# Kernel tuning notes

Measured on AMD Instinct MI355X. Metric: run time of the kernel, lower is better.

Reference implementation:

```python
import jax, jax.numpy as jnp
import numpy as np
from jax import lax

NEG = -9.0e15
ALPHA = 0.2  # LeakyReLU slope

def _cnn(x, conv1_w, conv1_b, conv2_w, conv2_b):
    # x: (BN,1,9,9)
    dn = ('NCHW', 'OIHW', 'NCHW')
    y = lax.conv_general_dilated(x, conv1_w, (1, 1), 'SAME', dimension_numbers=dn)
    y = jax.nn.relu(y + conv1_b[None, :, None, None])
    y = lax.conv_general_dilated(y, conv2_w, (1, 1), 'VALID', dimension_numbers=dn)
    y = jax.nn.relu(y + conv2_b[None, :, None, None])
    return y.reshape(y.shape[0], -1)  # (BN, 32*7*7=1568)

def _gat(h, adj, W, a1, a2):
    # h: (B,N,F) ; adj: (B,N,N) int
    Wh = h @ W                                  # (B,N,D)
    # a([Wh_i ; Wh_j]) == Wh_i@a1 + Wh_j@a2  (exact split of the concat linear)
    s1 = Wh @ a1                                # (B,N) query-node term
    s2 = Wh @ a2                                # (B,N) key-node term
    e = jax.nn.leaky_relu(s1[:, :, None] + s2[:, None, :], ALPHA)  # (B,N,N)
    e = jnp.where(adj > 0, e, NEG)
    attn = jax.nn.softmax(e, axis=-1)           # dropout off (eval mode)
    h_prime = jnp.einsum('bij,bjd->bid', attn, Wh)
    return jax.nn.elu(h_prime)

def reference(obs_grids, adj_matrix, conv1_w, conv1_b, conv2_w, conv2_b,
              W, a1, a2, actor_w, actor_b, critic_w, critic_b):
    B, N, C, H, Wd = obs_grids.shape
    feats = _cnn(obs_grids.reshape(B * N, C, H, Wd), conv1_w, conv1_b, conv2_w, conv2_b)
    feats = feats.reshape(B, N, -1)             # (B,N,1568)
    emb = _gat(feats, adj_matrix, W, a1, a2)    # (B,N,64)
    logits = emb @ actor_w + actor_b            # (B,N,n_actions)
    values = emb @ critic_w + critic_b          # (B,N,1)
    return (logits, values)

def setup_inputs() -> dict:
    key = jax.random.key(0)
    ks = jax.random.split(key, 12)
    B, N, H, Wd = 8, 1024, 9, 9
    FEAT, HID, NA = 1568, 64, 16
    f32 = jnp.float32
    inp = {}
    inp['obs_grids'] = jax.random.normal(ks[0], (B, N, 1, H, Wd), f32)
    inp['adj_matrix'] = jax.random.randint(ks[1], (B, N, N), 0, 2, jnp.int32)
    inp['conv1_w'] = jax.random.normal(ks[2], (16, 1, 3, 3), f32) * 0.1
    inp['conv1_b'] = jnp.zeros((16,), f32)
    inp['conv2_w'] = jax.random.normal(ks[3], (32, 16, 3, 3), f32) * 0.05
    inp['conv2_b'] = jnp.zeros((32,), f32)
    inp['W'] = jax.random.normal(ks[4], (FEAT, HID), f32) * (1.0 / np.sqrt(FEAT))
    inp['a1'] = jax.random.normal(ks[5], (HID,), f32) * 0.1
    inp['a2'] = jax.random.normal(ks[6], (HID,), f32) * 0.1
    inp['actor_w'] = jax.random.normal(ks[7], (HID, NA), f32) * (1.0 / np.sqrt(HID))
    inp['actor_b'] = jnp.zeros((NA,), f32)
    inp['critic_w'] = jax.random.normal(ks[8], (HID, 1), f32) * (1.0 / np.sqrt(HID))
    inp['critic_b'] = jnp.zeros((1,), f32)
    return inp
```

## Files before the change

kernel.cpp:

```cpp
#include <hip/hip_runtime.h>
#include <math.h>

#define NEG_BIG (-9.0e15f)

typedef __attribute__((ext_vector_type(8))) short short8;
typedef __attribute__((ext_vector_type(4))) float f32x4;

__device__ __forceinline__ short f32_to_bf16_bits(float f) {
  union { float f; unsigned u; } cv; cv.f = f;
  unsigned r = (cv.u + 0x7fffu + ((cv.u >> 16) & 1u)) >> 16;
  return (short)r;
}

__global__ __launch_bounds__(256) void wt_prep(const float* __restrict__ W,
                                               short* __restrict__ Wt) {
  int idx = blockIdx.x * 256 + threadIdx.x;
  if (idx < 1568 * 64) {
    int k = idx >> 6, n = idx & 63;
    Wt[n * 1568 + k] = f32_to_bf16_bits(W[idx]);
  }
}

#define IPB 8
#define FSTR 1608
__global__ __launch_bounds__(256) void cnn_gemm_kernel(
    const float* __restrict__ obs, const float* __restrict__ w1,
    const float* __restrict__ b1, const float* __restrict__ w2,
    const float* __restrict__ b2, const short* __restrict__ Wt,
    const float* __restrict__ a1, const float* __restrict__ a2,
    float* __restrict__ Wh, float* __restrict__ s1, float* __restrict__ s2)
{
  __shared__ float sw1[144];
  __shared__ float sb1[16];
  __shared__ float sb2[32];
  __shared__ __align__(16) short wt[32 * 160];
  __shared__ float sinp[IPB * 121];
  __shared__ __align__(16) short ubuf[IPB * FSTR];
  int tid = threadIdx.x;
  long inst0 = (long)blockIdx.x * IPB;

  for (int i = tid; i < 144; i += 256) sw1[i] = w1[i];
  if (tid < 16) sb1[tid] = b1[tid];
  if (tid < 32) sb2[tid] = b2[tid];
  for (int i = tid; i < 32 * 160; i += 256) {
    int o = i / 160, kp = i - o * 160;
    int kstep = kp >> 5, which = (kp >> 4) & 1, ci = kp & 15;
    int tap = kstep * 2 + which;
    float v = (tap < 9) ? w2[o * 144 + ci * 9 + tap] : 0.0f;
    wt[i] = f32_to_bf16_bits(v);
  }
  for (int i = tid; i < IPB * 121; i += 256) {
    int inst = i / 121, rem = i - inst * 121;
    int py = rem / 11, px = rem - py * 11;
    float v = 0.f;
    if (py >= 1 && py <= 9 && px >= 1 && px <= 9)
      v = obs[(inst0 + inst) * 81 + (py - 1) * 9 + (px - 1)];
    sinp[inst * 121 + rem] = v;
  }
  __syncthreads();

  {
    int inst = tid >> 5, s = tid & 31;
    const float* ib = &sinp[inst * 121];
    short* hw = &ubuf[inst * FSTR];
    for (int c = 0; c < 16; ++c) {
      float wk[9];
      #pragma unroll
      for (int k = 0; k < 9; ++k) wk[k] = sw1[c * 9 + k];
      float bias = sb1[c];
      #pragma unroll
      for (int t = 0; t < 3; ++t) {
        int px = s + t * 32;
        if (px < 81) {
          int y = (px * 456) >> 12;
          const float* ip = ib + px + 2 * y;
          float a = bias
            + ip[0]  * wk[0] + ip[1]  * wk[1] + ip[2]  * wk[2]
            + ip[11] * wk[3] + ip[12] * wk[4] + ip[13] * wk[5]
            + ip[22] * wk[6] + ip[23] * wk[7] + ip[24] * wk[8];
          a = fmaxf(a, 0.f);
          int idx = (px * 16 + c) ^ (((px >> 2) & 3) << 3);
          hw[idx] = f32_to_bf16_bits(a);
        }
      }
    }
  }

  int lane = tid & 63;
  int wv = tid >> 6;
  int g = lane >> 4;
  int which = g >> 1;
  int half = g & 1;
  int colr = lane & 15;

  const int offtab[9] = {0, 1, 2, 9, 10, 11, 18, 19, 20};
  int myoff[5];
  #pragma unroll
  for (int k = 0; k < 5; ++k) {
    int tap = k * 2 + which;
    myoff[k] = (tap < 9) ? offtab[tap] : 0;
  }
  int posm[4];
  #pragma unroll
  for (int mt = 0; mt < 4; ++mt) {
    int p = mt * 16 + colr;
    posm[mt] = (p < 49) ? (p / 7) * 9 + (p % 7) : 0;
  }
  short8 bfw[2][5];
  #pragma unroll
  for (int nt = 0; nt < 2; ++nt)
    #pragma unroll
    for (int k = 0; k < 5; ++k)
      bfw[nt][k] = *(const short8*)&wt[(nt * 16 + colr) * 160 + k * 32 + g * 8];

  #pragma unroll
  for (int ii = 0; ii < 2; ++ii) {
    int inst = wv * 2 + ii;
    const short* hb = &ubuf[inst * FSTR];
    short* fb = &ubuf[inst * FSTR];
    f32x4 acc[4][2];
    #pragma unroll
    for (int mt = 0; mt < 4; ++mt) {
      short8 af[5];
      #pragma unroll
      for (int k = 0; k < 5; ++k) {
        int row = posm[mt] + myoff[k];
        int idx = (row * 16 + half * 8) ^ (((row >> 2) & 3) << 3);
        af[k] = *(const short8*)&hb[idx];
      }
      #pragma unroll
      for (int nt = 0; nt < 2; ++nt) {
        f32x4 a0 = {0.f, 0.f, 0.f, 0.f};
        #pragma unroll
        for (int k = 0; k < 5; ++k)
          a0 = __builtin_amdgcn_mfma_f32_16x16x32_bf16(af[k], bfw[nt][k], a0, 0, 0, 0);
        acc[mt][nt] = a0;
      }
    }
    #pragma unroll
    for (int mt = 0; mt < 4; ++mt) {
      #pragma unroll
      for (int nt = 0; nt < 2; ++nt) {
        int o = nt * 16 + colr;
        float bias = sb2[o];
        #pragma unroll
        for (int r = 0; r < 4; ++r) {
          int p = mt * 16 + g * 4 + r;
          if (p < 49)
            fb[o * 49 + p] = f32_to_bf16_bits(fmaxf(acc[mt][nt][r] + bias, 0.f));
        }
      }
    }
  }
  __syncthreads();

  {
    int arow = colr & 7;
    const short* Wrow = Wt + (wv * 16 + colr) * 1568;
    f32x4 acc2 = {0.f, 0.f, 0.f, 0.f};
    for (int ks = 0; ks < 49; ++ks) {
      short8 af = *(const short8*)&ubuf[arow * FSTR + ks * 32 + g * 8];
      short8 bf = *(const short8*)&Wrow[ks * 32 + g * 8];
      acc2 = __builtin_amdgcn_mfma_f32_16x16x32_bf16(af, bf, acc2, 0, 0, 0);
    }
    float a1c = a1[wv * 16 + colr];
    float a2c = a2[wv * 16 + colr];
    float* sp1 = sinp;
    float* sp2 = sinp + 32;
    if (g < 2) {
      #pragma unroll
      for (int r = 0; r < 4; ++r) {
        int inst = g * 4 + r;
        float v = acc2[r];
        Wh[(inst0 + inst) * 64 + wv * 16 + colr] = v;
        float x1 = v * a1c, x2 = v * a2c;
        #pragma unroll
        for (int w = 1; w < 16; w <<= 1) { x1 += __shfl_xor(x1, w); x2 += __shfl_xor(x2, w); }
        if (colr == 0) { sp1[wv * 8 + inst] = x1; sp2[wv * 8 + inst] = x2; }
      }
    }
  }
  __syncthreads();
  if (tid < 8) {
    float* sp1 = sinp;
    float* sp2 = sinp + 32;
    s1[inst0 + tid] = sp1[tid] + sp1[8 + tid] + sp1[16 + tid] + sp1[24 + tid];
    s2[inst0 + tid] = sp2[tid] + sp2[8 + tid] + sp2[16 + tid] + sp2[24 + tid];
  }
}

#define PSTR 1028
__global__ __launch_bounds__(256) void gat_kernel(
    const int* __restrict__ adj, const float* __restrict__ Wh,
    const float* __restrict__ s1, const float* __restrict__ s2,
    const float* __restrict__ actor_w, const float* __restrict__ actor_b,
    const float* __restrict__ critic_w, const float* __restrict__ critic_b,
    float* __restrict__ out)
{
  __shared__ __align__(16) float p[16 * PSTR];
  __shared__ float s2s[1024];
  __shared__ float saw[64 * 16];
  __shared__ float scw[64];
  __shared__ float sab[16];
  __shared__ float denom[16];
  __shared__ float emb[16][65];
  int tid = threadIdx.x;
  int b = blockIdx.y;
  int i0 = blockIdx.x * 16;

  for (int j = tid; j < 1024; j += 256) s2s[j] = s2[b * 1024 + j];
  for (int idx2 = tid; idx2 < 64 * 16; idx2 += 256) saw[idx2] = actor_w[idx2];
  if (tid < 64) scw[tid] = critic_w[tid];
  if (tid < 16) sab[tid] = actor_b[tid];
  __syncthreads();

  {
    int il = tid >> 4, r = tid & 15;
    int i = i0 + il;
    float s1i = s1[b * 1024 + i];
    const int* arow = adj + ((long)(b * 1024 + i)) * 1024;
    float* prow = &p[il * PSTR];
    float m = -3.0e38f;
    for (int jj = 0; jj < 64; ++jj) {
      int j = r + jj * 16;
      int a = arow[j];
      float s = s1i + s2s[j];
      float e = (s > 0.f) ? s : 0.2f * s;
      e = (a > 0) ? e : NEG_BIG;
      prow[j] = e;
      m = fmaxf(m, e);
    }
    #pragma unroll
    for (int w = 1; w < 16; w <<= 1) m = fmaxf(m, __shfl_xor(m, w));
    float sum = 0.f;
    for (int jj = 0; jj < 64; ++jj) {
      int j = r + jj * 16;
      float pe = __expf(prow[j] - m);
      prow[j] = pe;
      sum += pe;
    }
    #pragma unroll
    for (int w = 1; w < 16; w <<= 1) sum += __shfl_xor(sum, w);
    if (r == 0) denom[il] = sum;
  }
  __syncthreads();

  int g = tid >> 6, sub = tid & 63, ti = sub >> 4, td = sub & 15;
  float acc[4][4] = {};
  const float* WhB = Wh + ((long)b * 1024) * 64;
  int k0 = g * 256;
  for (int k = k0; k < k0 + 256; k += 4) {
    float4 a4[4];
    #pragma unroll
    for (int ii = 0; ii < 4; ++ii) a4[ii] = *(const float4*)&p[(ti * 4 + ii) * PSTR + k];
    #pragma unroll
    for (int kk = 0; kk < 4; ++kk) {
      float4 wv2 = *(const float4*)&WhB[(k + kk) * 64 + td * 4];
      #pragma unroll
      for (int ii = 0; ii < 4; ++ii) {
        float av = (kk == 0) ? a4[ii].x : (kk == 1) ? a4[ii].y : (kk == 2) ? a4[ii].z : a4[ii].w;
        acc[ii][0] += av * wv2.x; acc[ii][1] += av * wv2.y;
        acc[ii][2] += av * wv2.z; acc[ii][3] += av * wv2.w;
      }
    }
  }
  __syncthreads();
  float* red = p;
  #pragma unroll
  for (int ii = 0; ii < 4; ++ii) {
    float4 v = {acc[ii][0], acc[ii][1], acc[ii][2], acc[ii][3]};
    *(float4*)&red[(g * 16 + ti * 4 + ii) * 64 + td * 4] = v;
  }
  __syncthreads();

  #pragma unroll
  for (int qq = 0; qq < 4; ++qq) {
    int q = tid + qq * 256;
    int il = q >> 6, d = q & 63;
    float v = red[il * 64 + d] + red[(16 + il) * 64 + d]
            + red[(32 + il) * 64 + d] + red[(48 + il) * 64 + d];
    v /= denom[il];
    v = (v > 0.f) ? v : expm1f(v);
    emb[il][d] = v;
  }
  __syncthreads();

  {
    int il = tid >> 4, na = tid & 15;
    float accl = sab[na];
    #pragma unroll
    for (int d = 0; d < 64; ++d) accl += emb[il][d] * saw[d * 16 + na];
    out[((long)(b * 1024 + i0 + il)) * 16 + na] = accl;
  }
  if (tid < 16) {
    float v = critic_b[0];
    #pragma unroll
    for (int d = 0; d < 64; ++d) v += emb[tid][d] * scw[d];
    out[131072 + b * 1024 + i0 + tid] = v;
  }
}

extern "C" void kernel_launch(void* const* d_in, const int* in_sizes, int n_in,
                              void* d_out, int out_size, void* d_ws, size_t ws_size,
                              hipStream_t stream)
{
  const float* obs = (const float*)d_in[0];
  const int*   adj = (const int*)d_in[1];
  const float* c1w = (const float*)d_in[2];
  const float* c1b = (const float*)d_in[3];
  const float* c2w = (const float*)d_in[4];
  const float* c2b = (const float*)d_in[5];
  const float* W   = (const float*)d_in[6];
  const float* a1  = (const float*)d_in[7];
  const float* a2  = (const float*)d_in[8];
  const float* aw  = (const float*)d_in[9];
  const float* ab  = (const float*)d_in[10];
  const float* cw  = (const float*)d_in[11];
  const float* cb  = (const float*)d_in[12];
  float* out = (float*)d_out;
  float* ws = (float*)d_ws;

  float* Wh  = ws;
  float* s1  = ws + 524288;
  float* s2  = s1 + 8192;
  short* Wt  = (short*)(s2 + 8192);

  hipLaunchKernelGGL(wt_prep, dim3((1568 * 64 + 255) / 256), dim3(256), 0, stream, W, Wt);
  hipLaunchKernelGGL(cnn_gemm_kernel, dim3(1024), dim3(256), 0, stream,
                     obs, c1w, c1b, c2w, c2b, Wt, a1, a2, Wh, s1, s2);
  hipLaunchKernelGGL(gat_kernel, dim3(64, 8), dim3(256), 0, stream,
                     adj, Wh, s1, s2, aw, ab, cw, cb, out);
}
```

Baseline: 80.19 us.

## Use bf16 MFMA for attention-weighted aggregation with transposed bf16 Wh

The CNN kernel now writes Wh as bf16 in a transposed (batch, feature, node) layout. The GAT kernel stores the softmax numerators as bf16 in shared memory and computes attn·Wh with 16x16x32 bf16 MFMA instead of the scalar FP32 outer-product loop and its cross-group reduction. The adjacency row is read with int4 loads into a per-thread bitmask and the logits are recomputed rather than staged in LDS. This halves Wh traffic and LDS use and removes a reduction pass, at the cost of bf16 rounding of the attention weights and Wh.

New measurement: 67.69 us. 1.18x faster.

```diff
diff --git a/kernel.cpp b/kernel.cpp
--- a/kernel.cpp
+++ b/kernel.cpp
@@ -4,6 +4,7 @@
 #define NEG_BIG (-9.0e15f)
 
 typedef __attribute__((ext_vector_type(8))) short short8;
+typedef __attribute__((ext_vector_type(4))) short short4v;
 typedef __attribute__((ext_vector_type(4))) float f32x4;
 
 __device__ __forceinline__ short f32_to_bf16_bits(float f) {
@@ -28,7 +29,7 @@
     const float* __restrict__ b1, const float* __restrict__ w2,
     const float* __restrict__ b2, const short* __restrict__ Wt,
     const float* __restrict__ a1, const float* __restrict__ a2,
-    float* __restrict__ Wh, float* __restrict__ s1, float* __restrict__ s2)
+    short* __restrict__ Whb, float* __restrict__ s1, float* __restrict__ s2)
 {
   __shared__ float sw1[144];
   __shared__ float sb1[16];
@@ -168,11 +169,16 @@
     float* sp1 = sinp;
     float* sp2 = sinp + 32;
     if (g < 2) {
+      long bidx = inst0 >> 10;
+      int node0 = (int)(inst0 & 1023) + g * 4;
+      short4v pk;
+      #pragma unroll
+      for (int r = 0; r < 4; ++r) pk[r] = f32_to_bf16_bits(acc2[r]);
+      *(short4v*)&Whb[(bidx * 64 + wv * 16 + colr) * 1024 + node0] = pk;
       #pragma unroll
       for (int r = 0; r < 4; ++r) {
         int inst = g * 4 + r;
         float v = acc2[r];
-        Wh[(inst0 + inst) * 64 + wv * 16 + colr] = v;
         float x1 = v * a1c, x2 = v * a2c;
         #pragma unroll
         for (int w = 1; w < 16; w <<= 1) { x1 += __shfl_xor(x1, w); x2 += __shfl_xor(x2, w); }
@@ -189,16 +195,16 @@
   }
 }
 
-#define PSTR 1028
+#define PSTR2 1096
 __global__ __launch_bounds__(256) void gat_kernel(
-    const int* __restrict__ adj, const float* __restrict__ Wh,
+    const int* __restrict__ adj, const short* __restrict__ Whb,
     const float* __restrict__ s1, const float* __restrict__ s2,
     const float* __restrict__ actor_w, const float* __restrict__ actor_b,
     const float* __restrict__ critic_w, const float* __restrict__ critic_b,
     float* __restrict__ out)
 {
-  __shared__ __align__(16) float p[16 * PSTR];
-  __shared__ float s2s[1024];
+  __shared__ __align__(16) short pb[16 * PSTR2];
+  __shared__ __align__(16) float s2s[1024];
   __shared__ float saw[64 * 16];
   __shared__ float scw[64];
   __shared__ float sab[16];
@@ -219,25 +225,43 @@
     int i = i0 + il;
     float s1i = s1[b * 1024 + i];
     const int* arow = adj + ((long)(b * 1024 + i)) * 1024;
-    float* prow = &p[il * PSTR];
+    unsigned long long amask = 0ull;
     float m = -3.0e38f;
-    for (int jj = 0; jj < 64; ++jj) {
-      int j = r + jj * 16;
-      int a = arow[j];
-      float s = s1i + s2s[j];
-      float e = (s > 0.f) ? s : 0.2f * s;
-      e = (a > 0) ? e : NEG_BIG;
-      prow[j] = e;
-      m = fmaxf(m, e);
+    #pragma unroll
+    for (int jj = 0; jj < 16; ++jj) {
+      int j0 = jj * 64 + r * 4;
+      int4 a4 = *(const int4*)&arow[j0];
+      float4 sv = *(const float4*)&s2s[j0];
+      float e0 = s1i + sv.x; e0 = (e0 > 0.f) ? e0 : 0.2f * e0;
+      float e1 = s1i + sv.y; e1 = (e1 > 0.f) ? e1 : 0.2f * e1;
+      float e2 = s1i + sv.z; e2 = (e2 > 0.f) ? e2 : 0.2f * e2;
+      float e3 = s1i + sv.w; e3 = (e3 > 0.f) ? e3 : 0.2f * e3;
+      if (a4.x > 0) { m = fmaxf(m, e0); amask |= 1ull << (jj * 4 + 0); }
+      if (a4.y > 0) { m = fmaxf(m, e1); amask |= 1ull << (jj * 4 + 1); }
+      if (a4.z > 0) { m = fmaxf(m, e2); amask |= 1ull << (jj * 4 + 2); }
+      if (a4.w > 0) { m = fmaxf(m, e3); amask |= 1ull << (jj * 4 + 3); }
     }
     #pragma unroll
     for (int w = 1; w < 16; w <<= 1) m = fmaxf(m, __shfl_xor(m, w));
     float sum = 0.f;
-    for (int jj = 0; jj < 64; ++jj) {
-      int j = r + jj * 16;
-      float pe = __expf(prow[j] - m);
-      prow[j] = pe;
-      sum += pe;
+    short* prow = &pb[il * PSTR2];
+    #pragma unroll
+    for (int jj = 0; jj < 16; ++jj) {
+      int j0 = jj * 64 + r * 4;
+      float4 sv = *(const float4*)&s2s[j0];
+      float e0 = s1i + sv.x; e0 = (e0 > 0.f) ? e0 : 0.2f * e0;
+      float e1 = s1i + sv.y; e1 = (e1 > 0.f) ? e1 : 0.2f * e1;
+      float e2 = s1i + sv.z; e2 = (e2 > 0.f) ? e2 : 0.2f * e2;
+      float e3 = s1i + sv.w; e3 = (e3 > 0.f) ? e3 : 0.2f * e3;
+      float p0 = ((amask >> (jj * 4 + 0)) & 1ull) ? __expf(e0 - m) : 0.f;
+      float p1 = ((amask >> (jj * 4 + 1)) & 1ull) ? __expf(e1 - m) : 0.f;
+      float p2 = ((amask >> (jj * 4 + 2)) & 1ull) ? __expf(e2 - m) : 0.f;
+      float p3 = ((amask >> (jj * 4 + 3)) & 1ull) ? __expf(e3 - m) : 0.f;
+      sum += (p0 + p1) + (p2 + p3);
+      short4v st;
+      st[0] = f32_to_bf16_bits(p0); st[1] = f32_to_bf16_bits(p1);
+      st[2] = f32_to_bf16_bits(p2); st[3] = f32_to_bf16_bits(p3);
+      *(short4v*)&prow[j0] = st;
     }
     #pragma unroll
     for (int w = 1; w < 16; w <<= 1) sum += __shfl_xor(sum, w);
@@ -245,43 +269,24 @@
   }
   __syncthreads();
 
-  int g = tid >> 6, sub = tid & 63, ti = sub >> 4, td = sub & 15;
-  float acc[4][4] = {};
-  const float* WhB = Wh + ((long)b * 1024) * 64;
-  int k0 = g * 256;
-  for (int k = k0; k < k0 + 256; k += 4) {
-    float4 a4[4];
-    #pragma unroll
-    for (int ii = 0; ii < 4; ++ii) a4[ii] = *(const float4*)&p[(ti * 4 + ii) * PSTR + k];
-    #pragma unroll
-    for (int kk = 0; kk < 4; ++kk) {
-      float4 wv2 = *(const float4*)&WhB[(k + kk) * 64 + td * 4];
-      #pragma unroll
-      for (int ii = 0; ii < 4; ++ii) {
-        float av = (kk == 0) ? a4[ii].x : (kk == 1) ? a4[ii].y : (kk == 2) ? a4[ii].z : a4[ii].w;
-        acc[ii][0] += av * wv2.x; acc[ii][1] += av * wv2.y;
-        acc[ii][2] += av * wv2.z; acc[ii][3] += av * wv2.w;
-      }
-    }
-  }
-  __syncthreads();
-  float* red = p;
-  #pragma unroll
-  for (int ii = 0; ii < 4; ++ii) {
-    float4 v = {acc[ii][0], acc[ii][1], acc[ii][2], acc[ii][3]};
-    *(float4*)&red[(g * 16 + ti * 4 + ii) * 64 + td * 4] = v;
-  }
-  __syncthreads();
-
-  #pragma unroll
-  for (int qq = 0; qq < 4; ++qq) {
-    int q = tid + qq * 256;
-    int il = q >> 6, d = q & 63;
-    float v = red[il * 64 + d] + red[(16 + il) * 64 + d]
-            + red[(32 + il) * 64 + d] + red[(48 + il) * 64 + d];
-    v /= denom[il];
-    v = (v > 0.f) ? v : expm1f(v);
-    emb[il][d] = v;
+  {
+    int lane = tid & 63, wv = tid >> 6, g = lane >> 4, colr = lane & 15;
+    const short* Wcol = Whb + ((long)b * 64 + wv * 16 + colr) * 1024;
+    const short* prow = &pb[colr * PSTR2];
+    f32x4 acc = {0.f, 0.f, 0.f, 0.f};
+    #pragma unroll
+    for (int ks = 0; ks < 32; ++ks) {
+      short8 af = *(const short8*)&prow[ks * 32 + g * 8];
+      short8 bf = *(const short8*)&Wcol[ks * 32 + g * 8];
+      acc = __builtin_amdgcn_mfma_f32_16x16x32_bf16(af, bf, acc, 0, 0, 0);
+    }
+    #pragma unroll
+    for (int rr = 0; rr < 4; ++rr) {
+      int row = g * 4 + rr;
+      float v = acc[rr] / denom[row];
+      v = (v > 0.f) ? v : expm1f(v);
+      emb[row][wv * 16 + colr] = v;
+    }
   }
   __syncthreads();
 
@@ -320,14 +325,14 @@
   float* out = (float*)d_out;
   float* ws = (float*)d_ws;
 
-  float* Wh  = ws;
-  float* s1  = ws + 524288;
+  short* Whb = (short*)ws;
+  float* s1  = ws + 262144;
   float* s2  = s1 + 8192;
   short* Wt  = (short*)(s2 + 8192);
 
   hipLaunchKernelGGL(wt_prep, dim3((1568 * 64 + 255) / 256), dim3(256), 0, stream, W, Wt);
   hipLaunchKernelGGL(cnn_gemm_kernel, dim3(1024), dim3(256), 0, stream,
-                     obs, c1w, c1b, c2w, c2b, Wt, a1, a2, Wh, s1, s2);
+                     obs, c1w, c1b, c2w, c2b, Wt, a1, a2, Whb, s1, s2);
   hipLaunchKernelGGL(gat_kernel, dim3(64, 8), dim3(256), 0, stream,
-                     adj, Wh, s1, s2, aw, ab, cw, cb, out);
-}
+                     adj, Whb, s1, s2, aw, ab, cw, cb, out);
+}
```
